# Kernel tuning notes

Measured on AMD Instinct MI355X. Metric: run time of the kernel, lower is better.

Reference implementation:

```python
import jax, jax.numpy as jnp
import numpy as np
import math

D_MODEL = 1024
H = 16
D_K = D_MODEL // H
D_FF = 4096
NEG = -1e9


def layer_norm(x, alpha, bias):
    # Faithful to source: mean over last dim, UNBIASED std (torch.std default),
    # eps defined in source but never used in forward.
    mean = jnp.mean(x, axis=-1, keepdims=True)
    std = jnp.std(x, axis=-1, ddof=1, keepdims=True)
    return (x - mean) / std * alpha + bias


def mha(x, mask, w_q, w_k, w_v, w_o):
    B, S, D = x.shape
    q = (x @ w_q.T).reshape(B, S, H, D_K)
    k = (x @ w_k.T).reshape(B, S, H, D_K)
    v = (x @ w_v.T).reshape(B, S, H, D_K)
    scores = jnp.einsum('bqhd,bkhd->bhqk', q, k) / math.sqrt(D_K)
    scores = jnp.where(mask, NEG, scores)
    attn = jax.nn.softmax(scores, axis=-1)
    out = jnp.einsum('bhqk,bkhd->bqhd', attn, v).reshape(B, S, D)
    return out @ w_o.T


def setup_inputs() -> dict:
    key = jax.random.key(0)
    ks = jax.random.split(key, 16)
    B, S = 4, 2048
    s = 0.02
    return {
        'x': jax.random.normal(ks[0], (B, S, D_MODEL), jnp.float32),
        'w_q': jax.random.normal(ks[1], (D_MODEL, D_MODEL), jnp.float32) * s,
        'w_k': jax.random.normal(ks[2], (D_MODEL, D_MODEL), jnp.float32) * s,
        'w_v': jax.random.normal(ks[3], (D_MODEL, D_MODEL), jnp.float32) * s,
        'w_o': jax.random.normal(ks[4], (D_MODEL, D_MODEL), jnp.float32) * s,
        'l1_w': jax.random.normal(ks[5], (D_FF, D_MODEL), jnp.float32) * s,
        'l1_b': jnp.zeros((D_FF,), jnp.float32),
        'l2_w': jax.random.normal(ks[6], (D_MODEL, D_FF), jnp.float32) * s,
        'l2_b': jnp.zeros((D_MODEL,), jnp.float32),
        'norm1_a': jnp.ones((D_MODEL,), jnp.float32),
        'norm1_b': jnp.zeros((D_MODEL,), jnp.float32),
        'norm2_a': jnp.ones((D_MODEL,), jnp.float32),
        'norm2_b': jnp.zeros((D_MODEL,), jnp.float32),
        'normf_a': jnp.ones((D_MODEL,), jnp.float32),
        'normf_b': jnp.zeros((D_MODEL,), jnp.float32),
        'mask': jax.random.randint(ks[7], (B, 1, 1, S), 0, 2) == 1,
    }


def reference(x, w_q, w_k, w_v, w_o, l1_w, l1_b, l2_w, l2_b,
              norm1_a, norm1_b, norm2_a, norm2_b, normf_a, normf_b, mask):
    # residual 1: pre-norm self-attention (dropout is identity at eval)
    x = x + mha(layer_norm(x, norm1_a, norm1_b), mask, w_q, w_k, w_v, w_o)
    # residual 2: pre-norm FFN
    h = layer_norm(x, norm2_a, norm2_b)
    ff = jax.nn.relu(h @ l1_w.T + l1_b) @ l2_w.T + l2_b
    x = x + ff
    return layer_norm(x, normf_a, normf_b)
```

## Files before the change

kernel.cpp:

```cpp
#include <hip/hip_runtime.h>
#include <hip/hip_bf16.h>


typedef __bf16 bf16x8 __attribute__((ext_vector_type(8)));
typedef float f32x4 __attribute__((ext_vector_type(4)));
typedef unsigned short u16x8 __attribute__((ext_vector_type(8)));
using bf16 = __hip_bfloat16;

__device__ __forceinline__ f32x4 mfma16(bf16x8 a, bf16x8 b, f32x4 c) {
  return __builtin_amdgcn_mfma_f32_16x16x32_bf16(a, b, c, 0, 0, 0);
}

__device__ __forceinline__ int swz(int row, int blk) {
  return row * 64 + ((blk ^ (row & 7)) << 3);
}

__device__ __forceinline__ void stage_tile64(unsigned short* lds,
                                             const bf16* g, int ld, int rows) {
  const int lane = threadIdx.x & 63, wid = threadIdx.x >> 6;
  const int r8 = lane >> 3, blk = lane & 7;
  const bf16* gl = g + (size_t)r8 * ld + ((blk ^ r8) << 3);
  const int passes = rows >> 3;
  for (int p = wid; p < passes; p += 4) {
    __builtin_amdgcn_global_load_lds(
        (const __attribute__((address_space(1))) void*)(gl + (size_t)(p * 8) * ld),
        (__attribute__((address_space(3))) void*)(lds + p * 512),
        16, 0, 0);
  }
}

__device__ __forceinline__ void stage_half512(unsigned short* lds,
                                              const bf16* g, int ld) {
  const int lane = threadIdx.x & 63, w8 = threadIdx.x >> 6;
  const int r8 = lane >> 3, blk = lane & 7;
  const bf16* gl = g + (size_t)r8 * ld + ((blk ^ r8) << 3);
  __builtin_amdgcn_global_load_lds(
      (const __attribute__((address_space(1))) void*)(gl + (size_t)(w8 * 8) * ld),
      (__attribute__((address_space(3))) void*)(lds + w8 * 512), 16, 0, 0);
  __builtin_amdgcn_global_load_lds(
      (const __attribute__((address_space(1))) void*)(gl + (size_t)((w8 + 8) * 8) * ld),
      (__attribute__((address_space(3))) void*)(lds + (w8 + 8) * 512), 16, 0, 0);
}

__device__ __forceinline__ short bfb(float x) {
  return (short)__hip_bfloat16_raw(__float2bfloat16(x)).x;
}

__global__ __launch_bounds__(256) void cvt_k(const float* __restrict__ s,
                                             bf16* __restrict__ d, int n) {
  const int i = (blockIdx.x * 256 + threadIdx.x) * 4;
  if (i + 3 < n) {
    const float4 v = *reinterpret_cast<const float4*>(s + i);
    ushort4 o;
    o.x = (unsigned short)bfb(v.x);
    o.y = (unsigned short)bfb(v.y);
    o.z = (unsigned short)bfb(v.z);
    o.w = (unsigned short)bfb(v.w);
    *reinterpret_cast<ushort4*>(d + i) = o;
  }
}

template <bool OUT_F32>
__global__ __launch_bounds__(256) void layernorm_k(const float* __restrict__ in,
                                                   const float* __restrict__ gamma,
                                                   const float* __restrict__ beta,
                                                   void* __restrict__ out) {
  __shared__ float red[8];
  const int row = blockIdx.x, t = threadIdx.x;
  const float4 vv = reinterpret_cast<const float4*>(in + (size_t)row * 1024)[t];
  const float x0 = vv.x, x1 = vv.y, x2 = vv.z, x3 = vv.w;
  float s = x0 + x1 + x2 + x3;
#pragma unroll
  for (int off = 32; off; off >>= 1) s += __shfl_down(s, off);
  if ((t & 63) == 0) red[t >> 6] = s;
  __syncthreads();
  const float mean = (red[0] + red[1] + red[2] + red[3]) * (1.0f / 1024.0f);
  const float d0 = x0 - mean, d1 = x1 - mean, d2 = x2 - mean, d3 = x3 - mean;
  float sq = d0 * d0 + d1 * d1 + d2 * d2 + d3 * d3;
#pragma unroll
  for (int off = 32; off; off >>= 1) sq += __shfl_down(sq, off);
  if ((t & 63) == 0) red[4 + (t >> 6)] = sq;
  __syncthreads();
  const float var =
      fmaxf((red[4] + red[5] + red[6] + red[7]) * (1.0f / 1023.0f), 1e-20f);
  const float rstd = rsqrtf(var);
  const float4 ga = reinterpret_cast<const float4*>(gamma)[t];
  const float4 be = reinterpret_cast<const float4*>(beta)[t];
  const float y0 = d0 * rstd * ga.x + be.x;
  const float y1 = d1 * rstd * ga.y + be.y;
  const float y2 = d2 * rstd * ga.z + be.z;
  const float y3 = d3 * rstd * ga.w + be.w;
  if (OUT_F32) {
    reinterpret_cast<float4*>((float*)out + (size_t)row * 1024)[t] =
        make_float4(y0, y1, y2, y3);
  } else {
    ushort4 o;
    o.x = (unsigned short)bfb(y0);
    o.y = (unsigned short)bfb(y1);
    o.z = (unsigned short)bfb(y2);
    o.w = (unsigned short)bfb(y3);
    reinterpret_cast<ushort4*>((bf16*)out + (size_t)row * 1024)[t] = o;
  }
}

template <bool HAS_BIAS, bool RELU, bool HAS_RES, bool OUT_F32>
__global__ __launch_bounds__(256) void gemm_bt(const bf16* __restrict__ A,
                                               const bf16* __restrict__ W,
                                               const float* __restrict__ bias,
                                               const float* __restrict__ resid,
                                               void* __restrict__ out,
                                               int M, int N, int K,
                                               int lda, int ldw) {
  __shared__ __align__(16) unsigned short As[128 * 64];
  __shared__ __align__(16) unsigned short Bs[128 * 64];
  const int lane = threadIdx.x & 63, wid = threadIdx.x >> 6;
  const int n16 = lane & 15, quad = lane >> 4;
  const int wm = (wid >> 1) * 64, wn = (wid & 1) * 64;
  const int tm = blockIdx.x * 128, tn = blockIdx.y * 128;
  f32x4 acc[4][4] = {};
  for (int k0 = 0; k0 < K; k0 += 64) {
    stage_tile64(As, A + (size_t)tm * lda + k0, lda, 128);
    stage_tile64(Bs, W + (size_t)tn * ldw + k0, ldw, 128);
    __syncthreads();
#pragma unroll
    for (int kk = 0; kk < 64; kk += 32) {
      bf16x8 af[4], bw[4];
#pragma unroll
      for (int i = 0; i < 4; ++i)
        af[i] = *reinterpret_cast<const bf16x8*>(
            &As[swz(wm + i * 16 + n16, (kk >> 3) + quad)]);
#pragma unroll
      for (int j = 0; j < 4; ++j)
        bw[j] = *reinterpret_cast<const bf16x8*>(
            &Bs[swz(wn + j * 16 + n16, (kk >> 3) + quad)]);
#pragma unroll
      for (int i = 0; i < 4; ++i)
#pragma unroll
        for (int j = 0; j < 4; ++j) acc[i][j] = mfma16(af[i], bw[j], acc[i][j]);
    }
    __syncthreads();
  }
#pragma unroll
  for (int i = 0; i < 4; ++i) {
#pragma unroll
    for (int j = 0; j < 4; ++j) {
      const int n = tn + wn + j * 16 + n16;
      const float bv = HAS_BIAS ? bias[n] : 0.0f;
#pragma unroll
      for (int r = 0; r < 4; ++r) {
        const int m = tm + wm + i * 16 + quad * 4 + r;
        float vv = acc[i][j][r] + bv;
        if (RELU) vv = fmaxf(vv, 0.0f);
        if (HAS_RES) vv += resid[(size_t)m * N + n];
        if (OUT_F32)
          ((float*)out)[(size_t)m * N + n] = vv;
        else
          ((bf16*)out)[(size_t)m * N + n] = __float2bfloat16(vv);
      }
    }
  }
}

#define PHASE(BUFSEL, Q, DO_B, STAGE_STMT, WAIT_STMT)                          \
  {                                                                            \
    const unsigned short* LA = Lds + (BUFSEL)*32768 + lasel * 8192;            \
    if (DO_B) {                                                                \
      const unsigned short* LB =                                               \
          Lds + (BUFSEL)*32768 + 16384 + lbsel * 8192;                         \
      _Pragma("unroll") for (int j = 0; j < 4; ++j) {                          \
        const int br = bloc + j * 16 + n16;                                    \
        bfr[j][0] = *reinterpret_cast<const bf16x8*>(&LB[swz(br, quad)]);      \
        bfr[j][1] = *reinterpret_cast<const bf16x8*>(&LB[swz(br, 4 + quad)]);  \
      }                                                                        \
    }                                                                          \
    bf16x8 a0[2], a1[2];                                                       \
    _Pragma("unroll") for (int ii = 0; ii < 2; ++ii) {                         \
      const int ar = ((Q)*2 + ii) * 16 + n16;                                  \
      a0[ii] = *reinterpret_cast<const bf16x8*>(&LA[swz(ar, quad)]);           \
      a1[ii] = *reinterpret_cast<const bf16x8*>(&LA[swz(ar, 4 + quad)]);       \
    }                                                                          \
    STAGE_STMT;                                                                \
    WAIT_STMT;                                                                 \
    __builtin_amdgcn_sched_barrier(0);                                         \
    __builtin_amdgcn_s_barrier();                                              \
    asm volatile("s_waitcnt lgkmcnt(0)" ::: "memory");                         \
    __builtin_amdgcn_sched_barrier(0);                                         \
    __builtin_amdgcn_s_setprio(1);                                             \
    _Pragma("unroll") for (int ii = 0; ii < 2; ++ii)                           \
        _Pragma("unroll") for (int j = 0; j < 4; ++j) {                        \
      f32x4 c = acc[(Q)*2 + ii][j];                                            \
      c = mfma16(a0[ii], bfr[j][0], c);                                        \
      c = mfma16(a1[ii], bfr[j][1], c);                                        \
      acc[(Q)*2 + ii][j] = c;                                                  \
    }                                                                          \
    __builtin_amdgcn_s_setprio(0);                                             \
    __builtin_amdgcn_sched_barrier(0);                                         \
    __builtin_amdgcn_s_barrier();                                              \
  }

template <bool QKV, bool HAS_BIAS, bool RELU>
__global__ __launch_bounds__(512, 2) void gemm256_k(
    const bf16* __restrict__ A0p, const bf16* __restrict__ cln,
    const bf16* __restrict__ W, const float* __restrict__ bias,
    const int* __restrict__ cnt, bf16* __restrict__ out,
    bf16* __restrict__ kvout, int M, int N, int K, int lda, int ldw) {
  __shared__ __align__(16) unsigned short Lds[65536];
  const int tm = blockIdx.x * 256;
  const int tn = blockIdx.y * 256;
  const bf16* A = A0p;
  bool isQ = true;
  if (QKV) {
    isQ = (blockIdx.y < 4);
    if (!isQ) {
      const int npad = (cnt[tm >> 11] + 127) & ~127;
      if ((tm & 2047) >= npad) return;
      A = cln;
    }
  }
  const int lane = threadIdx.x & 63, w8 = threadIdx.x >> 6;
  const int n16 = lane & 15, quad = lane >> 4;
  const int wm = (w8 >> 2) << 7;
  const int wn = (w8 & 3) << 6;
  const int lasel = wm >> 7, lbsel = wn >> 7, bloc = wn & 127;
  const int NTT = K >> 6;
  const bf16* Ag = A + (size_t)tm * lda;
  const bf16* Wg = W + (size_t)tn * ldw;
  f32x4 acc[8][4] = {};

  auto STAGE = [&](int bufsel, int region, int tile) {
    unsigned short* dst = Lds + bufsel * 32768 + region * 8192;
    if (region < 2)
      stage_half512(dst, Ag + (size_t)(region * 128) * lda + tile * 64, lda);
    else
      stage_half512(dst, Wg + (size_t)((region - 2) * 128) * ldw + tile * 64,
                    ldw);
  };

  STAGE(0, 0, 0); STAGE(0, 1, 0); STAGE(0, 2, 0); STAGE(0, 3, 0);
  STAGE(1, 2, 1); STAGE(1, 3, 1);
  asm volatile("s_waitcnt vmcnt(4)" ::: "memory");
  __builtin_amdgcn_sched_barrier(0);
  __builtin_amdgcn_s_barrier();

  for (int i = 0; i < NTT; i += 2) {
    const bool hasNext = (i + 2 < NTT);
    bf16x8 bfr[4][2];
    PHASE(0, 0, true, STAGE(1, 0, i + 1), );
    PHASE(0, 1, false, STAGE(1, 1, i + 1), );
    PHASE(0, 2, false, if (hasNext) STAGE(0, 2, i + 2), );
    PHASE(0, 3, false, if (hasNext) STAGE(0, 3, i + 2),
          if (hasNext) { asm volatile("s_waitcnt vmcnt(4)" ::: "memory"); }
          else { asm volatile("s_waitcnt vmcnt(0)" ::: "memory"); });
    PHASE(1, 0, true, if (hasNext) STAGE(0, 0, i + 2), );
    PHASE(1, 1, false, if (hasNext) STAGE(0, 1, i + 2), );
    PHASE(1, 2, false, if (hasNext) STAGE(1, 2, i + 3), );
    PHASE(1, 3, false, if (hasNext) STAGE(1, 3, i + 3),
          if (hasNext) { asm volatile("s_waitcnt vmcnt(4)" ::: "memory"); });
  }
  bf16* op;
  int ldo, nc0;
  if (QKV && !isQ) {
    op = kvout; ldo = 2048; nc0 = tn - 1024;
  } else if (QKV) {
    op = out; ldo = 1024; nc0 = tn;
  } else {
    op = out; ldo = N; nc0 = tn;
  }
#pragma unroll
  for (int i = 0; i < 8; ++i) {
#pragma unroll
    for (int j = 0; j < 4; ++j) {
      const int n = nc0 + wn + j * 16 + n16;
      const float bv = HAS_BIAS ? bias[n] : 0.0f;
#pragma unroll
      for (int r = 0; r < 4; ++r) {
        const int m = tm + wm + i * 16 + quad * 4 + r;
        float vv = acc[i][j][r] + bv;
        if (RELU) vv = fmaxf(vv, 0.0f);
        op[(size_t)m * ldo + n] = __float2bfloat16(vv);
      }
    }
  }
}

__global__ __launch_bounds__(256) void prep_mask_k(const int* __restrict__ m,
                                                   float* __restrict__ mf,
                                                   int n) {
  __shared__ int s;
  if (threadIdx.x == 0) s = 0;
  __syncthreads();
  unsigned int acc = 0;
  for (int i = threadIdx.x; i < 512; i += 256)
    acc |= ((const unsigned int*)m)[i] & 0xFFFFFF00u;
  if (acc) atomicOr(&s, 1);
  __syncthreads();
  const bool bytes = (s != 0);
  const int i = blockIdx.x * 256 + threadIdx.x;
  if (i < n) {
    const int v = bytes ? (int)((const unsigned char*)m)[i] : m[i];
    mf[i] = v ? -1.4427e9f : 0.0f;
  }
}

__global__ __launch_bounds__(256) void scan_k(const float* __restrict__ maskf,
                                              float* __restrict__ cmask,
                                              int* __restrict__ idx,
                                              int* __restrict__ cnt) {
  __shared__ int wsum[4];
  const int b = blockIdx.x, t = threadIdx.x, lane = t & 63, w = t >> 6;
  const float* mrow = maskf + b * 2048;
  int keep[8], local = 0;
#pragma unroll
  for (int e = 0; e < 8; ++e) {
    keep[e] = (mrow[t * 8 + e] == 0.0f) ? 1 : 0;
    local += keep[e];
  }
  int inc = local;
#pragma unroll
  for (int off = 1; off < 64; off <<= 1) {
    int v = __shfl_up(inc, off);
    if (lane >= off) inc += v;
  }
  if (lane == 63) wsum[w] = inc;
  __syncthreads();
  int base = 0;
#pragma unroll
  for (int i = 0; i < 4; ++i)
    if (i < w) base += wsum[i];
  int p = base + inc - local;
#pragma unroll
  for (int e = 0; e < 8; ++e)
    if (keep[e]) idx[b * 2048 + p++] = t * 8 + e;
  const int total = wsum[0] + wsum[1] + wsum[2] + wsum[3];
  if (t == 0) cnt[b] = total;
  for (int i = t; i < 2048; i += 256)
    cmask[b * 2048 + i] = (i < total) ? 0.0f : -1.4427e9f;
}

__global__ __launch_bounds__(128) void gatherA_k(const bf16* __restrict__ ln1,
                                                 const int* __restrict__ idx,
                                                 const int* __restrict__ cnt,
                                                 bf16* __restrict__ cln) {
  const int b = blockIdx.x >> 11, j = blockIdx.x & 2047;
  const int n = cnt[b];
  const int npad = (n + 127) & ~127;
  if (j >= npad) return;
  u16x8* dst = reinterpret_cast<u16x8*>(cln + ((size_t)(b * 2048 + j)) * 1024);
  if (j < n) {
    const int s = idx[b * 2048 + j];
    const u16x8* src =
        reinterpret_cast<const u16x8*>(ln1 + ((size_t)(b * 2048 + s)) * 1024);
    dst[threadIdx.x] = src[threadIdx.x];
  } else {
    u16x8 z = {};
    dst[threadIdx.x] = z;
  }
}

__global__ __launch_bounds__(256) void attn_k(const bf16* __restrict__ q,
                                              const bf16* __restrict__ kv,
                                              const float* __restrict__ cmask,
                                              const int* __restrict__ cnt,
                                              bf16* __restrict__ out, int BHN) {
  __shared__ __align__(16) unsigned short Ks[2][64 * 64];
  __shared__ __align__(16) unsigned short Vs[2][64 * 72];
  const int lane = threadIdx.x & 63, wid = threadIdx.x >> 6;
  const int n16 = lane & 15, quad = lane >> 4;
  const int bid = blockIdx.x;
  const int bh = bid % BHN, qb = bid / BHN;
  const int b = bh >> 4, h = bh & 15;
  const bf16* qp0 = q + (size_t)b * 2048 * 1024 + h * 64;
  const bf16* kp0 = kv + (size_t)b * 2048 * 2048 + h * 64;
  const bf16* vp0 = kp0 + 1024;
  const float* mfb = cmask + b * 2048;
  const int cntb = cnt[b];
  const int nk = ((cntb + 63) >> 6) << 6;
  const int qrow0 = qb * 128 + wid * 32;

  bf16x8 qf[2][2];
#pragma unroll
  for (int g = 0; g < 2; ++g) {
    const bf16* qp = qp0 + (size_t)(qrow0 + g * 16 + n16) * 1024 + quad * 8;
    qf[g][0] = *reinterpret_cast<const bf16x8*>(qp);
    qf[g][1] = *reinterpret_cast<const bf16x8*>(qp + 32);
  }
  bf16x8 ones;
#pragma unroll
  for (int e = 0; e < 8; ++e) ones[e] = (__bf16)1.0f;
  f32x4 oacc[2][4] = {};
  f32x4 lacc[2] = {};
  const int prow = ((n16 >> 2) << 3) + (n16 & 3);
  const int vkey = lane, vdc = wid * 16;

  stage_tile64(Ks[0], kp0, 2048, 64);
  {
    const bf16* vp = vp0 + (size_t)vkey * 2048 + vdc;
    const u16x8 a = *reinterpret_cast<const u16x8*>(vp);
    const u16x8 bq = *reinterpret_cast<const u16x8*>(vp + 8);
#pragma unroll
    for (int e = 0; e < 8; ++e) {
      Vs[0][(vdc + e) * 72 + vkey] = a[e];
      Vs[0][(vdc + 8 + e) * 72 + vkey] = bq[e];
    }
  }
  int cur = 0;
  for (int kt = 0; kt < nk; kt += 64) {
    __syncthreads();
    const bool hasNext = (kt + 64 < nk);
    const bool fullTile = (kt + 64 <= cntb);
    u16x8 na = {}, nb = {};
    if (hasNext) {
      stage_tile64(Ks[cur ^ 1], kp0 + (size_t)(kt + 64) * 2048, 2048, 64);
      const bf16* vp = vp0 + (size_t)(kt + 64 + vkey) * 2048 + vdc;
      na = *reinterpret_cast<const u16x8*>(vp);
      nb = *reinterpret_cast<const u16x8*>(vp + 8);
    }
    const unsigned short* Kc = Ks[cur];
    const unsigned short* Vc = Vs[cur];
#pragma unroll
    for (int sub = 0; sub < 2; ++sub) {
      const int kb = sub * 32;
      bf16x8 aflo[2], afhi[2];
#pragma unroll
      for (int st = 0; st < 2; ++st) {
        const int row = kb + prow + st * 4;
        aflo[st] = *reinterpret_cast<const bf16x8*>(&Kc[swz(row, quad)]);
        afhi[st] = *reinterpret_cast<const bf16x8*>(&Kc[swz(row, 4 + quad)]);
      }
      __builtin_amdgcn_s_setprio(1);
      f32x4 z[2][2];
#pragma unroll
      for (int g = 0; g < 2; ++g)
#pragma unroll
        for (int st = 0; st < 2; ++st) {
          f32x4 zz = {};
          zz = mfma16(aflo[st], qf[g][0], zz);
          zz = mfma16(afhi[st], qf[g][1], zz);
          z[g][st] = zz;
        }
      __builtin_amdgcn_s_setprio(0);
      float4 m0 = make_float4(0.f, 0.f, 0.f, 0.f);
      float4 m1 = make_float4(0.f, 0.f, 0.f, 0.f);
      if (!fullTile) {
        m0 = *reinterpret_cast<const float4*>(mfb + kt + kb + quad * 8);
        m1 = *reinterpret_cast<const float4*>(mfb + kt + kb + quad * 8 + 4);
      }
      bf16x8 vf[4];
#pragma unroll
      for (int j = 0; j < 4; ++j)
        vf[j] = *reinterpret_cast<const bf16x8*>(
            &Vc[(j * 16 + n16) * 72 + kb + quad * 8]);
#pragma unroll
      for (int g = 0; g < 2; ++g) {
        bf16x8 pf;
#pragma unroll
        for (int r = 0; r < 4; ++r) {
          const float e0 = __builtin_amdgcn_exp2f(
              fmaf(z[g][0][r], 0.18033688f, ((const float*)&m0)[r]));
          const float e1 = __builtin_amdgcn_exp2f(
              fmaf(z[g][1][r], 0.18033688f, ((const float*)&m1)[r]));
          pf[r] = (__bf16)e0;
          pf[4 + r] = (__bf16)e1;
        }
        __builtin_amdgcn_s_setprio(1);
#pragma unroll
        for (int j = 0; j < 4; ++j) oacc[g][j] = mfma16(pf, vf[j], oacc[g][j]);
        lacc[g] = mfma16(pf, ones, lacc[g]);
        __builtin_amdgcn_s_setprio(0);
      }
    }
    if (hasNext) {
      unsigned short* Vn = Vs[cur ^ 1];
#pragma unroll
      for (int e = 0; e < 8; ++e) {
        Vn[(vdc + e) * 72 + vkey] = na[e];
        Vn[(vdc + 8 + e) * 72 + vkey] = nb[e];
      }
    }
    cur ^= 1;
  }
#pragma unroll
  for (int g = 0; g < 2; ++g) {
#pragma unroll
    for (int r = 0; r < 4; ++r) {
      const float lr = 1.0f / fmaxf(lacc[g][r], 1e-20f);
      bf16* op =
          out + (size_t)(b * 2048 + qrow0 + g * 16 + quad * 4 + r) * 1024 +
          h * 64;
#pragma unroll
      for (int j = 0; j < 4; ++j)
        op[j * 16 + n16] = __float2bfloat16(oacc[g][j][r] * lr);
    }
  }
}

extern "C" void kernel_launch(void* const* d_in, const int* in_sizes, int n_in,
                              void* d_out, int out_size, void* d_ws,
                              size_t ws_size, hipStream_t stream) {
  const float* x    = (const float*)d_in[0];
  const float* w_q  = (const float*)d_in[1];
  const float* w_k  = (const float*)d_in[2];
  const float* w_v  = (const float*)d_in[3];
  const float* w_o  = (const float*)d_in[4];
  const float* l1_w = (const float*)d_in[5];
  const float* l1_b = (const float*)d_in[6];
  const float* l2_w = (const float*)d_in[7];
  const float* l2_b = (const float*)d_in[8];
  const float* n1a  = (const float*)d_in[9];
  const float* n1b  = (const float*)d_in[10];
  const float* n2a  = (const float*)d_in[11];
  const float* n2b  = (const float*)d_in[12];
  const float* nfa  = (const float*)d_in[13];
  const float* nfb  = (const float*)d_in[14];
  const int* mask   = (const int*)d_in[15];

  const int D = 1024, FF = 4096;
  const int M = in_sizes[0] / D;
  const int B = M / 2048;

  const size_t MB = 1024ull * 1024ull;
  if (ws_size < 121 * MB) return;
  char* w = (char*)d_ws;
  bf16* WQKV = (bf16*)(w + 0 * MB);
  bf16* WO   = (bf16*)(w + 6 * MB);
  bf16* L1W  = (bf16*)(w + 8 * MB);
  bf16* L2W  = (bf16*)(w + 16 * MB);
  bf16* LN1  = (bf16*)(w + 24 * MB);
  bf16* Qbuf = (bf16*)(w + 40 * MB);
  bf16* ATT  = LN1;
  bf16* HLN  = (bf16*)(w + 40 * MB);
  bf16* CLN  = (bf16*)(w + 56 * MB);
  bf16* FF1  = (bf16*)(w + 56 * MB);
  bf16* KV   = (bf16*)(w + 88 * MB);
  float* X1  = (float*)(w + 88 * MB);
  float* MASKF = (float*)(w + 120 * MB);
  float* CMASK = (float*)(w + 120 * MB + 256 * 1024);
  int*   IDX   = (int*)(w + 120 * MB + 512 * 1024);
  int*   CNT   = (int*)(w + 120 * MB + 768 * 1024);

  const dim3 blk(256);
  cvt_k<<<dim3(D * D / 1024), blk, 0, stream>>>(w_q, WQKV, D * D);
  cvt_k<<<dim3(D * D / 1024), blk, 0, stream>>>(w_k, WQKV + D * D, D * D);
  cvt_k<<<dim3(D * D / 1024), blk, 0, stream>>>(w_v, WQKV + 2 * D * D, D * D);
  cvt_k<<<dim3(D * D / 1024), blk, 0, stream>>>(w_o, WO, D * D);
  cvt_k<<<dim3(FF * D / 1024), blk, 0, stream>>>(l1_w, L1W, FF * D);
  cvt_k<<<dim3(FF * D / 1024), blk, 0, stream>>>(l2_w, L2W, FF * D);
  prep_mask_k<<<dim3((M + 255) / 256), blk, 0, stream>>>(mask, MASKF, M);
  scan_k<<<dim3(B), blk, 0, stream>>>(MASKF, CMASK, IDX, CNT);

  layernorm_k<false><<<M, blk, 0, stream>>>(x, n1a, n1b, LN1);
  gatherA_k<<<dim3(B * 2048), dim3(128), 0, stream>>>(LN1, IDX, CNT, CLN);
  gemm256_k<true, false, false><<<dim3(M / 256, 12), dim3(512), 0, stream>>>(
      LN1, CLN, WQKV, nullptr, CNT, Qbuf, KV, M, 3072, 1024, 1024, 1024);
  const int BHN = B * 16;
  attn_k<<<dim3((M / 128) * 16), blk, 0, stream>>>(Qbuf, KV, CMASK, CNT, ATT,
                                                   BHN);
  gemm_bt<false, false, true, true><<<dim3(M / 128, D / 128), blk, 0, stream>>>(
      ATT, WO, nullptr, x, X1, M, D, D, D, D);
  layernorm_k<false><<<M, blk, 0, stream>>>(X1, n2a, n2b, HLN);
  for (int c = 0; c < 2; ++c) {
    gemm256_k<false, true, true><<<dim3(M / 256, 8), dim3(512), 0, stream>>>(
        HLN, nullptr, L1W + (size_t)c * 2048 * D, l1_b + c * 2048, nullptr,
        FF1, nullptr, M, 2048, 1024, 1024, 1024);
    if (c == 0)
      gemm_bt<true, false, true, true>
          <<<dim3(M / 128, D / 128), blk, 0, stream>>>(
              FF1, L2W + c * 2048, l2_b, X1, X1, M, D, 2048, 2048, FF);
    else
      gemm_bt<false, false, true, true>
          <<<dim3(M / 128, D / 128), blk, 0, stream>>>(
              FF1, L2W + c * 2048, nullptr, X1, X1, M, D, 2048, 2048, FF);
  }
  layernorm_k<true><<<M, blk, 0, stream>>>(X1, nfa, nfb, (float*)d_out);
}
```

Before: 504.9 us.

## Merge GEMM pipeline phases in pairs and remap attention blocks across XCDs

The 256x256 GEMM main loop drops from eight phases to four per pair of k-tiles. Each merged phase loads four A fragments, issues two staging loads and runs twice the MFMAs between barriers, which halves the number of s_barrier synchronisations. The attention kernel's block index is permuted so that consecutive hardware blocks, which land on different XCDs, are regrouped and each XCD works on whole (batch, head) groups for better L2 reuse of K/V. The cost is more live fragment registers under launch_bounds(512,2), which risks spills, and coarser overlap between staging and compute.

```diff
diff --git a/kernel.cpp b/kernel.cpp
--- a/kernel.cpp
+++ b/kernel.cpp
@@ -161,7 +161,7 @@
   }
 }
 
-#define PHASE(BUFSEL, Q, DO_B, STAGE_STMT, WAIT_STMT)                          \
+#define PHASE2(BUFSEL, QB, DO_B, STAGES, WAITS)                                \
   {                                                                            \
     const unsigned short* LA = Lds + (BUFSEL)*32768 + lasel * 8192;            \
     if (DO_B) {                                                                \
@@ -173,25 +173,25 @@
         bfr[j][1] = *reinterpret_cast<const bf16x8*>(&LB[swz(br, 4 + quad)]);  \
       }                                                                        \
     }                                                                          \
-    bf16x8 a0[2], a1[2];                                                       \
-    _Pragma("unroll") for (int ii = 0; ii < 2; ++ii) {                         \
-      const int ar = ((Q)*2 + ii) * 16 + n16;                                  \
+    bf16x8 a0[4], a1[4];                                                       \
+    _Pragma("unroll") for (int ii = 0; ii < 4; ++ii) {                         \
+      const int ar = ((QB)*2 + ii) * 16 + n16;                                 \
       a0[ii] = *reinterpret_cast<const bf16x8*>(&LA[swz(ar, quad)]);           \
       a1[ii] = *reinterpret_cast<const bf16x8*>(&LA[swz(ar, 4 + quad)]);       \
     }                                                                          \
-    STAGE_STMT;                                                                \
-    WAIT_STMT;                                                                 \
+    STAGES;                                                                    \
+    WAITS;                                                                     \
     __builtin_amdgcn_sched_barrier(0);                                         \
     __builtin_amdgcn_s_barrier();                                              \
     asm volatile("s_waitcnt lgkmcnt(0)" ::: "memory");                         \
     __builtin_amdgcn_sched_barrier(0);                                         \
     __builtin_amdgcn_s_setprio(1);                                             \
-    _Pragma("unroll") for (int ii = 0; ii < 2; ++ii)                           \
+    _Pragma("unroll") for (int ii = 0; ii < 4; ++ii)                           \
         _Pragma("unroll") for (int j = 0; j < 4; ++j) {                        \
-      f32x4 c = acc[(Q)*2 + ii][j];                                            \
+      f32x4 c = acc[(QB)*2 + ii][j];                                           \
       c = mfma16(a0[ii], bfr[j][0], c);                                        \
       c = mfma16(a1[ii], bfr[j][1], c);                                        \
-      acc[(Q)*2 + ii][j] = c;                                                  \
+      acc[(QB)*2 + ii][j] = c;                                                 \
     }                                                                          \
     __builtin_amdgcn_s_setprio(0);                                             \
     __builtin_amdgcn_sched_barrier(0);                                         \
@@ -245,17 +245,16 @@
   for (int i = 0; i < NTT; i += 2) {
     const bool hasNext = (i + 2 < NTT);
     bf16x8 bfr[4][2];
-    PHASE(0, 0, true, STAGE(1, 0, i + 1), );
-    PHASE(0, 1, false, STAGE(1, 1, i + 1), );
-    PHASE(0, 2, false, if (hasNext) STAGE(0, 2, i + 2), );
-    PHASE(0, 3, false, if (hasNext) STAGE(0, 3, i + 2),
-          if (hasNext) { asm volatile("s_waitcnt vmcnt(4)" ::: "memory"); }
-          else { asm volatile("s_waitcnt vmcnt(0)" ::: "memory"); });
-    PHASE(1, 0, true, if (hasNext) STAGE(0, 0, i + 2), );
-    PHASE(1, 1, false, if (hasNext) STAGE(0, 1, i + 2), );
-    PHASE(1, 2, false, if (hasNext) STAGE(1, 2, i + 3), );
-    PHASE(1, 3, false, if (hasNext) STAGE(1, 3, i + 3),
-          if (hasNext) { asm volatile("s_waitcnt vmcnt(4)" ::: "memory"); });
+    PHASE2(0, 0, true, { STAGE(1, 0, i + 1); STAGE(1, 1, i + 1); }, );
+    PHASE2(0, 2, false,
+           if (hasNext) { STAGE(0, 2, i + 2); STAGE(0, 3, i + 2); },
+           if (hasNext) { asm volatile("s_waitcnt vmcnt(4)" ::: "memory"); }
+           else { asm volatile("s_waitcnt vmcnt(0)" ::: "memory"); });
+    PHASE2(1, 0, true,
+           if (hasNext) { STAGE(0, 0, i + 2); STAGE(0, 1, i + 2); }, );
+    PHASE2(1, 2, false,
+           if (hasNext && i + 3 < NTT) { STAGE(1, 2, i + 3); STAGE(1, 3, i + 3); },
+           if (hasNext) { asm volatile("s_waitcnt vmcnt(4)" ::: "memory"); });
   }
   bf16* op;
   int ldo, nc0;
@@ -366,8 +365,10 @@
   __shared__ __align__(16) unsigned short Vs[2][64 * 72];
   const int lane = threadIdx.x & 63, wid = threadIdx.x >> 6;
   const int n16 = lane & 15, quad = lane >> 4;
-  const int bid = blockIdx.x;
-  const int bh = bid % BHN, qb = bid / BHN;
+  const int bid0 = blockIdx.x;
+  const int nwg = gridDim.x;
+  const int bid = (bid0 & 7) * (nwg >> 3) + (bid0 >> 3);
+  const int qb = bid & 15, bh = bid >> 4;
   const int b = bh >> 4, h = bh & 15;
   const bf16* qp0 = q + (size_t)b * 2048 * 1024 + h * 64;
   const bf16* kp0 = kv + (size_t)b * 2048 * 2048 + h * 64;
```

After: 504.8 us. About the same (-0.0%).
